# Performance work log

Measured on AMD Instinct MI355X. Metric: run time of the kernel, lower is better.

Reference implementation:

```python
import jax, jax.numpy as jnp
import numpy as np

B, S, D = 2, 2048, 2048
H = 16
HD = D // H  # 128


def setup_inputs() -> dict:
    key = jax.random.key(0)
    ks = jax.random.split(key, 9)
    s = 1.0 / np.sqrt(D)
    return {
        "hidden_states": jax.random.normal(ks[0], (B, S, D), dtype=jnp.float32),
        "Wq": jax.random.normal(ks[1], (D, D), dtype=jnp.float32) * s,
        "bq": jnp.zeros((D,), dtype=jnp.float32),
        "Wk": jax.random.normal(ks[2], (D, D), dtype=jnp.float32) * s,
        "bk": jnp.zeros((D,), dtype=jnp.float32),
        "Wv": jax.random.normal(ks[3], (D, D), dtype=jnp.float32) * s,
        "bv": jnp.zeros((D,), dtype=jnp.float32),
        "Wo": jax.random.normal(ks[4], (D, D), dtype=jnp.float32) * s,
        "bo": jnp.zeros((D,), dtype=jnp.float32),
    }


def reference(hidden_states, Wq, bq, Wk, bk, Wv, bv, Wo, bo):
    x = hidden_states
    # linear projections (torch Linear: x @ W.T + b)
    q = x @ Wq.T + bq
    k = x @ Wk.T + bk
    v = x @ Wv.T + bv
    # [B, S, H, HD] -> [B, H, S, HD]
    q = q.reshape(B, S, H, HD).transpose(0, 2, 1, 3)
    k = k.reshape(B, S, H, HD).transpose(0, 2, 1, 3)
    v = v.reshape(B, S, H, HD).transpose(0, 2, 1, 3)
    q = q / jnp.sqrt(jnp.float32(HD))
    # scores [B, H, S, S]
    scores = jnp.einsum("bhqd,bhkd->bhqk", q, k)
    causal = jnp.triu(jnp.full((S, S), -jnp.inf, dtype=scores.dtype), k=1)
    scores = scores + causal
    attn = jax.nn.softmax(scores, axis=-1)
    out = jnp.einsum("bhqk,bhkd->bhqd", attn, v)
    out = out.transpose(0, 2, 1, 3).reshape(B, S, D)
    return out @ Wo.T + bo
```

## Files before the change

kernel.cpp:

```cpp
#include <hip/hip_runtime.h>
#include <stdint.h>

#define S_LEN 2048
#define DMODEL 2048
#define NHEAD 16
#define HDIM 128

typedef __attribute__((ext_vector_type(8))) short short8;
typedef __attribute__((ext_vector_type(4))) float floatx4;

__device__ __forceinline__ unsigned short f2b(float f) {
  union { float f; unsigned u; } v; v.f = f;
  unsigned r = v.u + 0x7FFFu + ((v.u >> 16) & 1u);
  return (unsigned short)(r >> 16);
}

__device__ __forceinline__ void load_lds16(const unsigned short* g, unsigned short* l) {
  __builtin_amdgcn_global_load_lds((const __attribute__((address_space(1))) void*)g,
                                   (__attribute__((address_space(3))) void*)l, 16, 0, 0);
}

__global__ __launch_bounds__(256) void cvt_all(const float* __restrict__ x,
                                               const float* __restrict__ Wq, const float* __restrict__ Wk,
                                               const float* __restrict__ Wv, const float* __restrict__ Wo,
                                               unsigned short* __restrict__ xb,
                                               unsigned short* __restrict__ Wqb, unsigned short* __restrict__ Wkb,
                                               unsigned short* __restrict__ Wvb, unsigned short* __restrict__ Wob) {
  const size_t idx = (size_t)blockIdx.x * 256 + threadIdx.x;
  const int y = blockIdx.y;
  const float4* s; ushort4* d;
  if (y == 0)      { s = (const float4*)x;               d = (ushort4*)xb; }
  else if (y == 1) { s = (const float4*)x + (1u << 20);  d = (ushort4*)xb + (1u << 20); }
  else if (y == 2) { s = (const float4*)Wq;              d = (ushort4*)Wqb; }
  else if (y == 3) { s = (const float4*)Wk;              d = (ushort4*)Wkb; }
  else if (y == 4) { s = (const float4*)Wv;              d = (ushort4*)Wvb; }
  else             { s = (const float4*)Wo;              d = (ushort4*)Wob; }
  float4 f = s[idx];
  ushort4 o;
  o.x = f2b(f.x); o.y = f2b(f.y); o.z = f2b(f.z); o.w = f2b(f.w);
  d[idx] = o;
}


#define REG256(buf, op, ks) (lds + ((((buf)*2 + (op)) * 2 + (ks)) * 8192))
#define STAGE256(buf, op, ks, kt)                                                    \
  do {                                                                               \
    unsigned short* _d = REG256(buf, op, ks);                                        \
    const unsigned short* _g0 = ((op) ? gB[0] : gA[0]) + (kt) * 64 + (ks) * 32;      \
    const unsigned short* _g1 = ((op) ? gB[1] : gA[1]) + (kt) * 64 + (ks) * 32;      \
    load_lds16(_g0, _d + ldso[0]);                                                   \
    load_lds16(_g1, _d + ldso[1]);                                                   \
  } while (0)
#define RDA256(buf, ks)                                                              \
  { _Pragma("unroll") for (int mf = 0; mf < 8; mf++)                                 \
      av[mf] = *(const short8*)(REG256(buf, 0, ks) + aoff + mf * 512); }
#define RDB256(buf, ks, nh)                                                          \
  { bv[0] = *(const short8*)(REG256(buf, 1, ks) + boff + (nh) * 1024);               \
    bv[1] = *(const short8*)(REG256(buf, 1, ks) + boff + (nh) * 1024 + 512); }
#define MFMACL256(nh)                                                                \
  { __builtin_amdgcn_s_setprio(1);                                                   \
    _Pragma("unroll") for (int mf = 0; mf < 8; mf++) {                               \
      acc[mf][(nh)*2]   = __builtin_amdgcn_mfma_f32_16x16x32_bf16(av[mf], bv[0], acc[mf][(nh)*2],   0, 0, 0); \
      acc[mf][(nh)*2+1] = __builtin_amdgcn_mfma_f32_16x16x32_bf16(av[mf], bv[1], acc[mf][(nh)*2+1], 0, 0, 0); } \
    __builtin_amdgcn_s_setprio(0); }
#define BAR256 __builtin_amdgcn_s_barrier()
#define LGKM0 asm volatile("s_waitcnt lgkmcnt(0)" ::: "memory")
#define VMC4 asm volatile("s_waitcnt vmcnt(4)" ::: "memory")
#define VMC0 asm volatile("s_waitcnt vmcnt(0)" ::: "memory")

__device__ __forceinline__ void gemm256_body(const unsigned short* __restrict__ A,
                                             const unsigned short* __restrict__ Bw,
                                             const float* __restrict__ bias,
                                             void* __restrict__ out, int mode, float scale,
                                             int m0, int n0, unsigned short* lds) {
  const int K = DMODEL;
  const int t = threadIdx.x;
  const int lane = t & 63, w = t >> 6;
  const int quad = lane >> 4, lc = lane & 15;
  const int wm = w >> 2, wn = w & 3;

  const int chunkoff = ((lane & 3) ^ ((lane >> 3) & 3)) * 8;
  const unsigned short* gA[2];
  const unsigned short* gB[2];
  int ldso[2];
#pragma unroll
  for (int i = 0; i < 2; i++) {
    const int c = w * 2 + i;
    const int r = c * 16 + (lane >> 2);
    gA[i] = A + (size_t)(m0 + r) * K + chunkoff;
    gB[i] = Bw + (size_t)(n0 + r) * K + chunkoff;
    ldso[i] = c * 512 + lane * 8;
  }

  const int rsw = ((lc >> 1) & 3);
  const int aoff = (wm * 128 + lc) * 32 + ((quad ^ rsw) * 8);
  const int boff = (wn * 64 + lc) * 32 + ((quad ^ rsw) * 8);

  floatx4 acc[8][4] = {};
  short8 av[8], bv[2];

  STAGE256(0, 0, 0, 0); STAGE256(0, 1, 0, 0); STAGE256(0, 0, 1, 0); STAGE256(0, 1, 1, 0);
  STAGE256(1, 0, 0, 1); STAGE256(1, 1, 0, 1);
  VMC4;
  BAR256;

  const int NKT = K / 64;
  const int NIT = NKT / 2;
  for (int it = 0; it < NIT; it++) {
    const int kt1 = 2 * it + 1;
    const int kt2 = (2 * it + 2 < NKT) ? 2 * it + 2 : NKT - 1;
    const int kt3 = (2 * it + 3 < NKT) ? 2 * it + 3 : NKT - 1;
    RDA256(0, 0); RDB256(0, 0, 0); STAGE256(1, 0, 1, kt1); BAR256; LGKM0; MFMACL256(0); BAR256;
    RDB256(0, 0, 1);               STAGE256(1, 1, 1, kt1); BAR256; LGKM0; MFMACL256(1); BAR256;
    RDA256(0, 1); RDB256(0, 1, 0); STAGE256(0, 0, 0, kt2); BAR256; LGKM0; MFMACL256(0); BAR256;
    RDB256(0, 1, 1);               STAGE256(0, 1, 0, kt2); BAR256; LGKM0; MFMACL256(1); VMC4; BAR256;
    RDA256(1, 0); RDB256(1, 0, 0); STAGE256(0, 0, 1, kt2); BAR256; LGKM0; MFMACL256(0); BAR256;
    RDB256(1, 0, 1);               STAGE256(0, 1, 1, kt2); BAR256; LGKM0; MFMACL256(1); BAR256;
    RDA256(1, 1); RDB256(1, 1, 0); STAGE256(1, 0, 0, kt3); BAR256; LGKM0; MFMACL256(0); BAR256;
    RDB256(1, 1, 1);               STAGE256(1, 1, 0, kt3); BAR256; LGKM0; MFMACL256(1); VMC4; BAR256;
  }

  VMC0;
  BAR256;

#pragma unroll
  for (int nf = 0; nf < 4; nf++) {
    const int col = n0 + wn * 64 + nf * 16 + lc;
    const float bcol = bias[col];
#pragma unroll
    for (int mf = 0; mf < 8; mf++) {
      const int row0 = m0 + wm * 128 + mf * 16 + quad * 4;
      if (mode == 1) {
        ushort4 o;
        o.x = f2b((acc[mf][nf][0] + bcol) * scale);
        o.y = f2b((acc[mf][nf][1] + bcol) * scale);
        o.z = f2b((acc[mf][nf][2] + bcol) * scale);
        o.w = f2b((acc[mf][nf][3] + bcol) * scale);
        const int b = row0 >> 11;
        const int s = row0 & (S_LEN - 1);
        *(ushort4*)&((unsigned short*)out)[((size_t)(b * DMODEL + col)) * S_LEN + s] = o;
      } else if (mode == 2) {
#pragma unroll
        for (int r = 0; r < 4; r++)
          ((float*)out)[(size_t)(row0 + r) * DMODEL + col] = (acc[mf][nf][r] + bcol) * scale;
      } else {
#pragma unroll
        for (int r = 0; r < 4; r++)
          ((unsigned short*)out)[(size_t)(row0 + r) * DMODEL + col] = f2b((acc[mf][nf][r] + bcol) * scale);
      }
    }
  }
}

__global__ __launch_bounds__(512, 2)
void qkv256(const unsigned short* __restrict__ xb,
            const unsigned short* __restrict__ Wqb, const unsigned short* __restrict__ Wkb,
            const unsigned short* __restrict__ Wvb,
            const float* __restrict__ bq, const float* __restrict__ bk, const float* __restrict__ bvp,
            unsigned short* __restrict__ Qb, unsigned short* __restrict__ Kb,
            unsigned short* __restrict__ Vtb, float qscale) {
  __shared__ unsigned short lds[65536];
  const int sel = blockIdx.x >> 3;
  const int n0 = (blockIdx.x & 7) * 256;
  const int m0 = blockIdx.y * 256;
  const unsigned short* Bw = (sel == 0) ? Wqb : (sel == 1) ? Wkb : Wvb;
  const float* bias = (sel == 0) ? bq : (sel == 1) ? bk : bvp;
  void* out = (sel == 0) ? (void*)Qb : (sel == 1) ? (void*)Kb : (void*)Vtb;
  const float scale = (sel == 0) ? qscale : 1.f;
  const int mode = (sel == 2) ? 1 : 0;
  gemm256_body(xb, Bw, bias, out, mode, scale, m0, n0, lds);
}

__global__ __launch_bounds__(512, 2)
void out256(const unsigned short* __restrict__ Ob, const unsigned short* __restrict__ Wob,
            const float* __restrict__ bo, float* __restrict__ out) {
  __shared__ unsigned short lds[65536];
  gemm256_body(Ob, Wob, bo, out, 2, 1.f, blockIdx.y * 256, blockIdx.x * 256, lds);
}

__global__ __launch_bounds__(256, 2)
void attn_fwd(const unsigned short* __restrict__ Qg, const unsigned short* __restrict__ Kg,
              const unsigned short* __restrict__ Vtg, unsigned short* __restrict__ Og) {
  __shared__ unsigned short Ks[2][64 * 128];
  __shared__ unsigned short Vs[128 * 64];
  __shared__ unsigned short Ps[128 * 72];

  const int t = threadIdx.x;
  const int lane = t & 63, w = t >> 6;
  const int quad = lane >> 4, lc = lane & 15;
  const int y = blockIdx.y;
  const int tile = (y < 16) ? (int)blockIdx.x : 15 - (int)blockIdx.x;
  const int b = y >> 4, h = y & 15;
  const size_t qkbase = (size_t)b * S_LEN * DMODEL + h * HDIM;
  const size_t vtbase = ((size_t)(b * DMODEL + h * HDIM)) * S_LEN;
  const int q0 = tile * 128;
  const int wrow = q0 + w * 32;

  short8 aq[2][4];
#pragma unroll
  for (int pm = 0; pm < 2; pm++)
#pragma unroll
    for (int ks = 0; ks < 4; ks++)
      aq[pm][ks] = *(const short8*)&Qg[qkbase + (size_t)(wrow + pm * 16 + lc) * DMODEL + ks * 32 + quad * 8];

  const unsigned short* kga[4];
  const unsigned short* vga[4];
  int kloff[4], vloff[4];
#pragma unroll
  for (int i = 0; i < 4; i++) {
    int c = w * 4 + i;
    int krow = 4 * c + (lane >> 4);
    kga[i] = Kg + qkbase + (size_t)krow * DMODEL + ((lane & 15) ^ (krow & 15)) * 8;
    kloff[i] = c * 512 + lane * 8;
    int vrow = 8 * c + (lane >> 3);
    vga[i] = Vtg + vtbase + (size_t)vrow * S_LEN + ((lane & 7) ^ (vrow & 7)) * 8;
    vloff[i] = c * 512 + lane * 8;
  }

  floatx4 oaccT[8][2] = {};
  float m_run[2] = {-1e30f, -1e30f}, l_run[2] = {0.f, 0.f};

  const int kiters = 2 * tile + 2;

#pragma unroll
  for (int i = 0; i < 4; i++) load_lds16(kga[i], &Ks[0][kloff[i]]);

  for (int kb = 0; kb < kiters; kb++) {
    const int k0 = kb * 64;
    const int cur = kb & 1;
    __syncthreads();

#pragma unroll
    for (int i = 0; i < 4; i++) load_lds16(vga[i] + k0, &Vs[vloff[i]]);
    {
      const size_t knext = (size_t)((kb + 1 < kiters) ? k0 + 64 : k0) * DMODEL;
#pragma unroll
      for (int i = 0; i < 4; i++) load_lds16(kga[i] + knext, &Ks[cur ^ 1][kloff[i]]);
    }

    const bool hasw = (k0 <= wrow + 31);
    float alpha[2];
    if (hasw) {
      floatx4 st[4][2];
#pragma unroll
      for (int mt = 0; mt < 4; mt++)
#pragma unroll
        for (int pm = 0; pm < 2; pm++) st[mt][pm] = (floatx4){0.f, 0.f, 0.f, 0.f};
#pragma unroll
      for (int ks = 0; ks < 4; ks++) {
        short8 kf[4];
#pragma unroll
        for (int mt = 0; mt < 4; mt++) {
          int n = mt * 16 + lc;
          kf[mt] = *(const short8*)&Ks[cur][n * 128 + (((ks * 4 + quad) ^ (n & 15)) * 8)];
        }
#pragma unroll
        for (int mt = 0; mt < 4; mt++)
#pragma unroll
          for (int pm = 0; pm < 2; pm++)
            st[mt][pm] = __builtin_amdgcn_mfma_f32_16x16x32_bf16(kf[mt], aq[pm][ks], st[mt][pm], 0, 0, 0);
      }

      float mx[2] = {-1e30f, -1e30f};
      if (k0 + 63 > wrow) {
#pragma unroll
        for (int pm = 0; pm < 2; pm++) {
          const int qq = wrow + pm * 16 + lc;
#pragma unroll
          for (int mt = 0; mt < 4; mt++) {
            const int key = k0 + mt * 16 + quad * 4;
#pragma unroll
            for (int r = 0; r < 4; r++) {
              if (key + r > qq) st[mt][pm][r] = -1e30f;
              mx[pm] = fmaxf(mx[pm], st[mt][pm][r]);
            }
          }
        }
      } else {
#pragma unroll
        for (int pm = 0; pm < 2; pm++)
#pragma unroll
          for (int mt = 0; mt < 4; mt++)
#pragma unroll
            for (int r = 0; r < 4; r++) mx[pm] = fmaxf(mx[pm], st[mt][pm][r]);
      }
#pragma unroll
      for (int pm = 0; pm < 2; pm++) {
        mx[pm] = fmaxf(mx[pm], __shfl_xor(mx[pm], 16));
        mx[pm] = fmaxf(mx[pm], __shfl_xor(mx[pm], 32));
        float mnew = fmaxf(m_run[pm], mx[pm]);
        alpha[pm] = __builtin_amdgcn_exp2f(m_run[pm] - mnew);
        m_run[pm] = mnew;
        l_run[pm] *= alpha[pm];
      }

#pragma unroll
      for (int pm = 0; pm < 2; pm++)
#pragma unroll
        for (int mt = 0; mt < 4; mt++) {
          float p0 = __builtin_amdgcn_exp2f(st[mt][pm][0] - m_run[pm]);
          float p1 = __builtin_amdgcn_exp2f(st[mt][pm][1] - m_run[pm]);
          float p2 = __builtin_amdgcn_exp2f(st[mt][pm][2] - m_run[pm]);
          float p3 = __builtin_amdgcn_exp2f(st[mt][pm][3] - m_run[pm]);
          l_run[pm] += (p0 + p1) + (p2 + p3);
          ushort4 o;
          o.x = f2b(p0); o.y = f2b(p1); o.z = f2b(p2); o.w = f2b(p3);
          *(ushort4*)&Ps[(w * 32 + pm * 16 + lc) * 72 + mt * 16 + quad * 4] = o;
        }
    }

    asm volatile("s_waitcnt vmcnt(4)\n\ts_barrier" ::: "memory");

    if (hasw) {
#pragma unroll
      for (int mt8 = 0; mt8 < 8; mt8++)
#pragma unroll
        for (int pm = 0; pm < 2; pm++) {
          oaccT[mt8][pm][0] *= alpha[pm]; oaccT[mt8][pm][1] *= alpha[pm];
          oaccT[mt8][pm][2] *= alpha[pm]; oaccT[mt8][pm][3] *= alpha[pm];
        }

#pragma unroll
      for (int ks = 0; ks < 2; ks++) {
        short8 pf[2];
#pragma unroll
        for (int pm = 0; pm < 2; pm++)
          pf[pm] = *(const short8*)&Ps[(w * 32 + pm * 16 + lc) * 72 + ks * 32 + quad * 8];
#pragma unroll
        for (int mt8 = 0; mt8 < 8; mt8++) {
          int n = mt8 * 16 + lc;
          short8 vf = *(const short8*)&Vs[n * 64 + (((ks * 4 + quad) ^ (n & 7)) * 8)];
#pragma unroll
          for (int pm = 0; pm < 2; pm++)
            oaccT[mt8][pm] = __builtin_amdgcn_mfma_f32_16x16x32_bf16(vf, pf[pm], oaccT[mt8][pm], 0, 0, 0);
        }
      }
    }
  }

#pragma unroll
  for (int pm = 0; pm < 2; pm++) {
    l_run[pm] += __shfl_xor(l_run[pm], 16);
    l_run[pm] += __shfl_xor(l_run[pm], 32);
    float inv = 1.f / l_run[pm];
    size_t obase = ((size_t)(b * S_LEN + wrow + pm * 16 + lc)) * DMODEL + h * HDIM;
#pragma unroll
    for (int mt8 = 0; mt8 < 8; mt8++) {
      ushort4 o;
      o.x = f2b(oaccT[mt8][pm][0] * inv);
      o.y = f2b(oaccT[mt8][pm][1] * inv);
      o.z = f2b(oaccT[mt8][pm][2] * inv);
      o.w = f2b(oaccT[mt8][pm][3] * inv);
      *(ushort4*)&Og[obase + mt8 * 16 + quad * 4] = o;
    }
  }
}

extern "C" void kernel_launch(void* const* d_in, const int* in_sizes, int n_in,
                              void* d_out, int out_size, void* d_ws, size_t ws_size,
                              hipStream_t stream) {
  const float* x  = (const float*)d_in[0];
  const float* Wq = (const float*)d_in[1];
  const float* bq = (const float*)d_in[2];
  const float* Wk = (const float*)d_in[3];
  const float* bk = (const float*)d_in[4];
  const float* Wv = (const float*)d_in[5];
  const float* bv = (const float*)d_in[6];
  const float* Wo = (const float*)d_in[7];
  const float* bo = (const float*)d_in[8];

  char* w = (char*)d_ws;
  unsigned short* xb  = (unsigned short*)(w);
  unsigned short* Wqb = (unsigned short*)(w + (size_t)16 * (1 << 20));
  unsigned short* Wkb = (unsigned short*)(w + (size_t)24 * (1 << 20));
  unsigned short* Wvb = (unsigned short*)(w + (size_t)32 * (1 << 20));
  unsigned short* Wob = (unsigned short*)(w + (size_t)40 * (1 << 20));
  unsigned short* Qb  = (unsigned short*)(w + (size_t)48 * (1 << 20));
  unsigned short* Kb  = (unsigned short*)(w + (size_t)64 * (1 << 20));
  unsigned short* Vtb = (unsigned short*)(w + (size_t)80 * (1 << 20));
  unsigned short* Ob  = (unsigned short*)(w + (size_t)96 * (1 << 20));

  cvt_all<<<dim3(4096, 6), 256, 0, stream>>>(x, Wq, Wk, Wv, Wo, xb, Wqb, Wkb, Wvb, Wob);

  const float qscale = 0.08838834764831843f * 1.4426950408889634f;
  qkv256<<<dim3(24, 16), 512, 0, stream>>>(xb, Wqb, Wkb, Wvb, bq, bk, bv, Qb, Kb, Vtb, qscale);

  attn_fwd<<<dim3(16, 32), 256, 0, stream>>>(Qb, Kb, Vtb, Ob);

  out256<<<dim3(8, 16), 512, 0, stream>>>(Ob, Wob, bo, (float*)d_out);
}
```

Before: 398.5 us.

## Double-buffer GEMM fragment registers to overlap LDS reads with MFMA

```diff
diff --git a/kernel.cpp b/kernel.cpp
--- a/kernel.cpp
+++ b/kernel.cpp
@@ -51,20 +51,19 @@
     load_lds16(_g0, _d + ldso[0]);                                                   \
     load_lds16(_g1, _d + ldso[1]);                                                   \
   } while (0)
-#define RDA256(buf, ks)                                                              \
+#define RDA_TO(dst, buf, ks)                                                         \
   { _Pragma("unroll") for (int mf = 0; mf < 8; mf++)                                 \
-      av[mf] = *(const short8*)(REG256(buf, 0, ks) + aoff + mf * 512); }
-#define RDB256(buf, ks, nh)                                                          \
-  { bv[0] = *(const short8*)(REG256(buf, 1, ks) + boff + (nh) * 1024);               \
-    bv[1] = *(const short8*)(REG256(buf, 1, ks) + boff + (nh) * 1024 + 512); }
-#define MFMACL256(nh)                                                                \
+      dst[mf] = *(const short8*)(REG256(buf, 0, ks) + aoff + mf * 512); }
+#define RDB_TO(dst, buf, ks, nh)                                                     \
+  { dst[0] = *(const short8*)(REG256(buf, 1, ks) + boff + (nh) * 1024);              \
+    dst[1] = *(const short8*)(REG256(buf, 1, ks) + boff + (nh) * 1024 + 512); }
+#define MFMA16(a, b, nh)                                                             \
   { __builtin_amdgcn_s_setprio(1);                                                   \
     _Pragma("unroll") for (int mf = 0; mf < 8; mf++) {                               \
-      acc[mf][(nh)*2]   = __builtin_amdgcn_mfma_f32_16x16x32_bf16(av[mf], bv[0], acc[mf][(nh)*2],   0, 0, 0); \
-      acc[mf][(nh)*2+1] = __builtin_amdgcn_mfma_f32_16x16x32_bf16(av[mf], bv[1], acc[mf][(nh)*2+1], 0, 0, 0); } \
+      acc[mf][(nh)*2]   = __builtin_amdgcn_mfma_f32_16x16x32_bf16(a[mf], b[0], acc[mf][(nh)*2],   0, 0, 0); \
+      acc[mf][(nh)*2+1] = __builtin_amdgcn_mfma_f32_16x16x32_bf16(a[mf], b[1], acc[mf][(nh)*2+1], 0, 0, 0); } \
     __builtin_amdgcn_s_setprio(0); }
 #define BAR256 __builtin_amdgcn_s_barrier()
-#define LGKM0 asm volatile("s_waitcnt lgkmcnt(0)" ::: "memory")
 #define VMC4 asm volatile("s_waitcnt vmcnt(4)" ::: "memory")
 #define VMC0 asm volatile("s_waitcnt vmcnt(0)" ::: "memory")
 
@@ -97,12 +96,14 @@
   const int boff = (wn * 64 + lc) * 32 + ((quad ^ rsw) * 8);
 
   floatx4 acc[8][4] = {};
-  short8 av[8], bv[2];
+  short8 av0[8], av1[8], bv0[2], bv1[2];
 
   STAGE256(0, 0, 0, 0); STAGE256(0, 1, 0, 0); STAGE256(0, 0, 1, 0); STAGE256(0, 1, 1, 0);
   STAGE256(1, 0, 0, 1); STAGE256(1, 1, 0, 1);
   VMC4;
   BAR256;
+  RDA_TO(av0, 0, 0);
+  RDB_TO(bv0, 0, 0, 0);
 
   const int NKT = K / 64;
   const int NIT = NKT / 2;
@@ -110,14 +111,46 @@
     const int kt1 = 2 * it + 1;
     const int kt2 = (2 * it + 2 < NKT) ? 2 * it + 2 : NKT - 1;
     const int kt3 = (2 * it + 3 < NKT) ? 2 * it + 3 : NKT - 1;
-    RDA256(0, 0); RDB256(0, 0, 0); STAGE256(1, 0, 1, kt1); BAR256; LGKM0; MFMACL256(0); BAR256;
-    RDB256(0, 0, 1);               STAGE256(1, 1, 1, kt1); BAR256; LGKM0; MFMACL256(1); BAR256;
-    RDA256(0, 1); RDB256(0, 1, 0); STAGE256(0, 0, 0, kt2); BAR256; LGKM0; MFMACL256(0); BAR256;
-    RDB256(0, 1, 1);               STAGE256(0, 1, 0, kt2); BAR256; LGKM0; MFMACL256(1); VMC4; BAR256;
-    RDA256(1, 0); RDB256(1, 0, 0); STAGE256(0, 0, 1, kt2); BAR256; LGKM0; MFMACL256(0); BAR256;
-    RDB256(1, 0, 1);               STAGE256(0, 1, 1, kt2); BAR256; LGKM0; MFMACL256(1); BAR256;
-    RDA256(1, 1); RDB256(1, 1, 0); STAGE256(1, 0, 0, kt3); BAR256; LGKM0; MFMACL256(0); BAR256;
-    RDB256(1, 1, 1);               STAGE256(1, 1, 0, kt3); BAR256; LGKM0; MFMACL256(1); VMC4; BAR256;
+    BAR256;
+    STAGE256(1, 0, 1, kt1);
+    RDB_TO(bv1, 0, 0, 1);
+    MFMA16(av0, bv0, 0);
+    BAR256;
+    STAGE256(1, 1, 1, kt1);
+    RDA_TO(av1, 0, 1);
+    RDB_TO(bv0, 0, 1, 0);
+    MFMA16(av0, bv1, 1);
+    VMC4;
+    BAR256;
+    STAGE256(0, 0, 0, kt2);
+    RDB_TO(bv1, 0, 1, 1);
+    MFMA16(av1, bv0, 0);
+    BAR256;
+    STAGE256(0, 1, 0, kt2);
+    RDA_TO(av0, 1, 0);
+    RDB_TO(bv0, 1, 0, 0);
+    MFMA16(av1, bv1, 1);
+    VMC4;
+    BAR256;
+    STAGE256(0, 0, 1, kt2);
+    RDB_TO(bv1, 1, 0, 1);
+    MFMA16(av0, bv0, 0);
+    BAR256;
+    STAGE256(0, 1, 1, kt2);
+    RDA_TO(av1, 1, 1);
+    RDB_TO(bv0, 1, 1, 0);
+    MFMA16(av0, bv1, 1);
+    VMC4;
+    BAR256;
+    STAGE256(1, 0, 0, kt3);
+    RDB_TO(bv1, 1, 1, 1);
+    MFMA16(av1, bv0, 0);
+    BAR256;
+    STAGE256(1, 1, 0, kt3);
+    RDA_TO(av0, 0, 0);
+    RDB_TO(bv0, 0, 0, 0);
+    MFMA16(av1, bv1, 1);
+    VMC4;
   }
 
   VMC0;
@@ -246,6 +279,7 @@
       for (int mt = 0; mt < 4; mt++)
 #pragma unroll
         for (int pm = 0; pm < 2; pm++) st[mt][pm] = (floatx4){0.f, 0.f, 0.f, 0.f};
+      __builtin_amdgcn_s_setprio(1);
 #pragma unroll
       for (int ks = 0; ks < 4; ks++) {
         short8 kf[4];
@@ -260,6 +294,7 @@
           for (int pm = 0; pm < 2; pm++)
             st[mt][pm] = __builtin_amdgcn_mfma_f32_16x16x32_bf16(kf[mt], aq[pm][ks], st[mt][pm], 0, 0, 0);
       }
+      __builtin_amdgcn_s_setprio(0);
 
       float mx[2] = {-1e30f, -1e30f};
       if (k0 + 63 > wrow) {
@@ -326,6 +361,7 @@
 #pragma unroll
         for (int pm = 0; pm < 2; pm++)
           pf[pm] = *(const short8*)&Ps[(w * 32 + pm * 16 + lc) * 72 + ks * 32 + quad * 8];
+        __builtin_amdgcn_s_setprio(1);
 #pragma unroll
         for (int mt8 = 0; mt8 < 8; mt8++) {
           int n = mt8 * 16 + lc;
@@ -334,6 +370,7 @@
           for (int pm = 0; pm < 2; pm++)
             oaccT[mt8][pm] = __builtin_amdgcn_mfma_f32_16x16x32_bf16(vf, pf[pm], oaccT[mt8][pm], 0, 0, 0);
         }
+        __builtin_amdgcn_s_setprio(0);
       }
     }
   }
```

New measurement: 479.4 us. +20.3%, slower.
